# Optimization experiments

Measured on AMD Instinct MI355X. Metric: run time of the kernel, lower is better.

The kernel has to match this reference:

```python
import jax, jax.numpy as jnp
import numpy as np

# SSMBlock constants (from init_kwargs and standard mamba_ssm defaults)
W = 8            # pooled spatial edge; d_model = W^3
K = 16           # AvgPool3d kernel & stride
D_MODEL = W ** 3            # 512
D_STATE = 16
EXPAND = 2
D_INNER = EXPAND * D_MODEL  # 1024
DT_RANK = D_MODEL // 16     # 32 (ceil(512/16))
D_CONV = 4


def setup_inputs() -> dict:
    key = jax.random.key(0)
    ks = jax.random.split(key, 8)
    s = 0.02
    x = jax.random.normal(ks[0], (1, 64, 128, 128, 128), dtype=jnp.float32)
    in_proj_w = jax.random.normal(ks[1], (2 * D_INNER, D_MODEL), jnp.float32) * s
    conv_w = jax.random.normal(ks[2], (D_INNER, D_CONV), jnp.float32) * s
    conv_b = jnp.zeros((D_INNER,), jnp.float32)
    x_proj_w = jax.random.normal(ks[3], (DT_RANK + 2 * D_STATE, D_INNER), jnp.float32) * s
    dt_proj_w = jax.random.normal(ks[4], (D_INNER, DT_RANK), jnp.float32) * s
    dt_proj_b = jax.random.uniform(ks[5], (D_INNER,), jnp.float32, minval=-4.0, maxval=-2.0)
    A_log = jnp.log(jnp.broadcast_to(jnp.arange(1, D_STATE + 1, dtype=jnp.float32), (D_INNER, D_STATE)))
    D = jnp.ones((D_INNER,), jnp.float32)
    out_proj_w = jax.random.normal(ks[6], (D_MODEL, D_INNER), jnp.float32) * s
    return dict(x=x, in_proj_w=in_proj_w, conv_w=conv_w, conv_b=conv_b,
                x_proj_w=x_proj_w, dt_proj_w=dt_proj_w, dt_proj_b=dt_proj_b,
                A_log=A_log, D=D, out_proj_w=out_proj_w)


def _forward(x, in_proj_w, conv_w, conv_b, x_proj_w, dt_proj_w, dt_proj_b, A_log, D, out_proj_w):
    B, C = x.shape[0], x.shape[1]
    # AvgPool3d(K, stride=K): non-overlapping -> reshape + mean
    xp = x.reshape(B, C, W, K, W, K, W, K).mean(axis=(3, 5, 7))  # (B,C,W,W,W)
    seq = xp.reshape(B, C, D_MODEL)  # Mamba input: L = C, d_model = W^3

    # in_proj -> (x, z)
    xz = jnp.einsum('bld,ed->ble', seq, in_proj_w)  # (B,L,2*D_INNER)
    xs, z = jnp.split(xz, 2, axis=-1)

    # causal depthwise conv1d along L + SiLU
    xt = jnp.pad(xs, ((0, 0), (D_CONV - 1, 0), (0, 0))).transpose(0, 2, 1)  # (B,E,L+pad)
    conv = jax.lax.conv_general_dilated(
        xt, conv_w[:, None, :], window_strides=(1,), padding='VALID',
        dimension_numbers=('NCH', 'OIH', 'NCH'), feature_group_count=D_INNER)
    xs = jax.nn.silu(conv.transpose(0, 2, 1) + conv_b)  # (B,L,E)

    # input-dependent dt, B, C
    x_dbl = jnp.einsum('ble,fe->blf', xs, x_proj_w)
    dt, Bs, Cs = jnp.split(x_dbl, [DT_RANK, DT_RANK + D_STATE], axis=-1)
    dt = jax.nn.softplus(jnp.einsum('blr,er->ble', dt, dt_proj_w) + dt_proj_b)  # (B,L,E)

    # selective scan: h_t = exp(dt*A) h_{t-1} + (dt*x) B_t ; y_t = <h_t, C_t> + D*x_t
    A = -jnp.exp(A_log)                                  # (E,S)
    dA = jnp.exp(dt[..., None] * A)                      # (B,L,E,S)
    dBx = (dt * xs)[..., None] * Bs[:, :, None, :]       # (B,L,E,S)

    def step(h, inp):
        da, dbx, c = inp
        h = da * h + dbx                                 # (B,E,S)
        y = jnp.einsum('bes,bs->be', h, c)
        return h, y

    h0 = jnp.zeros((B, D_INNER, D_STATE), xs.dtype)
    _, ys = jax.lax.scan(step, h0, (dA.transpose(1, 0, 2, 3), dBx.transpose(1, 0, 2, 3), Cs.transpose(1, 0, 2)))
    y = ys.transpose(1, 0, 2) + xs * D                   # (B,L,E)

    y = y * jax.nn.silu(z)
    out = jnp.einsum('ble,de->bld', y, out_proj_w)       # (B,L,d_model)
    return out.reshape(B, C, W, W, W)


def reference(x, in_proj_w, conv_w, conv_b, x_proj_w, dt_proj_w, dt_proj_b, A_log, D, out_proj_w):
    return _forward(x, in_proj_w, conv_w, conv_b, x_proj_w, dt_proj_w, dt_proj_b, A_log, D, out_proj_w)
```

## Files before the change

kernel.cpp:

```cpp
#include <hip/hip_runtime.h>
#include <math.h>

typedef float f32x4 __attribute__((ext_vector_type(4)));

__device__ __forceinline__ float dot4v(f32x4 a, f32x4 b){
    return a.x*b.x + a.y*b.y + a.z*b.z + a.w*b.w;
}
__device__ __forceinline__ float dot4(float4 a, float4 b){
    return a.x*b.x + a.y*b.y + a.z*b.z + a.w*b.w;
}

__device__ __forceinline__ float reduce4(float a0, float a1, float a2, float a3, int lane){
    int b0 = lane & 1, b1 = lane & 2;
    float r  = b0 ? a1 : a0;
    float rt = b0 ? a0 : a1;
    r += __shfl_xor(rt, 1);
    float s  = b0 ? a3 : a2;
    float st = b0 ? a2 : a3;
    s += __shfl_xor(st, 1);
    float u  = b1 ? s : r;
    float ut = b1 ? r : s;
    u += __shfl_xor(ut, 2);
    u += __shfl_xor(u, 4);
    u += __shfl_xor(u, 8);
    u += __shfl_xor(u, 16);
    u += __shfl_xor(u, 32);
    return u;
}

__global__ __launch_bounds__(256) void pool_k(const float* __restrict__ x,
                                              float* __restrict__ seq){
    __shared__ float red[4][8];
    int tid  = threadIdx.x;
    int lane = tid & 63;
    int part = tid >> 6;
    int cdh  = blockIdx.x;
    int c  = cdh >> 6;
    int od = (cdh >> 3) & 7;
    int oh = cdh & 7;
    int half = lane >> 5;
    int f    = lane & 31;

    const f32x4* px = (const f32x4*)x;
    size_t base = ((size_t)(c * 128 + od * 16) * 128 + (size_t)(oh * 16 + half)) * 32 + f
                + (size_t)part * 4 * 4096;

    float acc = 0.f;
    #pragma unroll
    for (int ii = 0; ii < 4; ii++){
        size_t o = base + (size_t)ii * 4096;
        #pragma unroll
        for (int jj = 0; jj < 8; jj++){
            f32x4 v = __builtin_nontemporal_load(&px[o + (size_t)jj * 64]);
            acc += (v.x + v.y) + (v.z + v.w);
        }
    }
    acc += __shfl_xor(acc, 1);
    acc += __shfl_xor(acc, 2);
    acc += __shfl_xor(acc, 32);
    if (lane < 32 && (lane & 3) == 0) red[part][lane >> 2] = acc;
    __syncthreads();
    if (tid < 8){
        float v = red[0][tid] + red[1][tid] + red[2][tid] + red[3][tid];
        seq[c * 512 + od * 64 + oh * 8 + tid] = v * (1.0f / 4096.0f);
    }
}

__global__ __launch_bounds__(256) void inproj_k(const float* __restrict__ seq,
                                                const float* __restrict__ Win,
                                                float* __restrict__ xz){
    int lane = threadIdx.x & 63;
    int wid  = blockIdx.x * 4 + (threadIdx.x >> 6);
    int l0 = (wid >> 7) << 3;
    int e0 = (wid & 127) << 4;
    const f32x4* S = (const f32x4*)seq;
    f32x4 sa[8], sb[8];
    #pragma unroll
    for (int r = 0; r < 8; r++){
        sa[r] = S[(size_t)(l0 + r) * 128 + lane];
        sb[r] = S[(size_t)(l0 + r) * 128 + lane + 64];
    }
    #pragma unroll 2
    for (int j = 0; j < 16; j++){
        int e = e0 + j;
        const f32x4* W = (const f32x4*)Win + (size_t)e * 128;
        f32x4 w0 = W[lane], w1 = W[lane + 64];
        float a[8];
        #pragma unroll
        for (int r = 0; r < 8; r++) a[r] = dot4v(w0, sa[r]) + dot4v(w1, sb[r]);
        float u0 = reduce4(a[0], a[1], a[2], a[3], lane);
        float u1 = reduce4(a[4], a[5], a[6], a[7], lane);
        if (lane < 4){
            xz[(size_t)(l0 + lane) * 2048 + e]     = u0;
            xz[(size_t)(l0 + 4 + lane) * 2048 + e] = u1;
        }
    }
}

__global__ __launch_bounds__(1024) void cxp_k(const float* __restrict__ xz,
                                              const float* __restrict__ cw,
                                              const float* __restrict__ cb,
                                              const float* __restrict__ Wx,
                                              float* __restrict__ xsT,
                                              float* __restrict__ zsT,
                                              float* __restrict__ bcT,
                                              float* __restrict__ xdT){
    __shared__ float xs_row[1024];
    int l = blockIdx.x;
    int t = threadIdx.x;

    {
        int e = t;
        float v = cb[e];
        #pragma unroll
        for (int tt = 0; tt < 4; tt++){
            int ll = l - 3 + tt;
            if (ll >= 0) v += cw[e * 4 + tt] * xz[(size_t)ll * 2048 + e];
        }
        v = v / (1.f + expf(-v));
        xs_row[e] = v;
        xsT[(size_t)e * 64 + l] = v;
        float zv = xz[(size_t)l * 2048 + 1024 + e];
        zsT[(size_t)e * 64 + l] = zv / (1.f + expf(-zv));
    }
    __syncthreads();

    {
        int f = t >> 4, q = t & 15;
        const float4* X  = (const float4*)xs_row;
        const float4* W4 = (const float4*)(Wx + (size_t)f * 1024);
        float acc = 0.f;
        #pragma unroll
        for (int k4 = 0; k4 < 16; k4++){
            int idx = q * 16 + k4;
            acc += dot4(X[idx], W4[idx]);
        }
        acc += __shfl_xor(acc, 1);
        acc += __shfl_xor(acc, 2);
        acc += __shfl_xor(acc, 4);
        acc += __shfl_xor(acc, 8);
        if (q == 0){
            if (f < 32) xdT[(size_t)f * 64 + l] = acc;
            else        bcT[(size_t)(f - 32) * 64 + l] = acc;
        }
    }
}

__global__ __launch_bounds__(256) void scan_k(const float* __restrict__ xdT,
                                              const float* __restrict__ bcT,
                                              const float* __restrict__ xsT,
                                              const float* __restrict__ zsT,
                                              const float* __restrict__ Wdt,
                                              const float* __restrict__ bdt,
                                              const float* __restrict__ A_log,
                                              const float* __restrict__ Dv,
                                              float* __restrict__ y){
    __shared__ float red[4][64];
    int e    = blockIdx.x;
    int lane = threadIdx.x & 63;
    int w    = threadIdx.x >> 6;

    float acc = bdt[e];
    #pragma unroll 8
    for (int k = 0; k < 32; k++) acc += xdT[k * 64 + lane] * Wdt[e * 32 + k];
    float dtv = (acc > 20.f) ? acc : log1pf(expf(acc));
    float xv  = xsT[(size_t)e * 64 + lane];

    float py = 0.f;
    #pragma unroll
    for (int i = 0; i < 4; i++){
        int s = w * 4 + i;
        float A = -expf(A_log[e * 16 + s]);
        float a = expf(dtv * A);
        float b = (dtv * xv) * bcT[s * 64 + lane];
        #pragma unroll
        for (int d = 1; d < 64; d <<= 1){
            float ap = __shfl_up(a, d);
            float bp = __shfl_up(b, d);
            if (lane >= d){ b += a * bp; a *= ap; }
        }
        py += b * bcT[(16 + s) * 64 + lane];
    }
    red[w][lane] = py;
    __syncthreads();
    if (threadIdx.x < 64){
        float tot = red[0][lane] + red[1][lane] + red[2][lane] + red[3][lane];
        float yv = (tot + xv * Dv[e]) * zsT[(size_t)e * 64 + lane];
        y[(size_t)lane * 1024 + e] = yv;
    }
}

__global__ __launch_bounds__(256) void outproj_k(const float* __restrict__ y,
                                                 const float* __restrict__ Wo,
                                                 float* __restrict__ out){
    int lane = threadIdx.x & 63;
    int wid  = blockIdx.x * 4 + (threadIdx.x >> 6);
    int l0 = (wid >> 5) << 2;
    int d0 = (wid & 31) << 4;
    const float4* Y = (const float4*)y;
    float4 y0[4], y1[4], y2[4], y3[4];
    #pragma unroll
    for (int q = 0; q < 4; q++){
        y0[q] = Y[(size_t)(l0+0)*256 + q*64 + lane];
        y1[q] = Y[(size_t)(l0+1)*256 + q*64 + lane];
        y2[q] = Y[(size_t)(l0+2)*256 + q*64 + lane];
        y3[q] = Y[(size_t)(l0+3)*256 + q*64 + lane];
    }
    #pragma unroll 2
    for (int j = 0; j < 16; j++){
        int d = d0 + j;
        const float4* W = (const float4*)Wo + (size_t)d * 256;
        float a0 = 0.f, a1 = 0.f, a2 = 0.f, a3 = 0.f;
        #pragma unroll
        for (int q = 0; q < 4; q++){
            float4 w = W[q * 64 + lane];
            a0 += dot4(w, y0[q]);
            a1 += dot4(w, y1[q]);
            a2 += dot4(w, y2[q]);
            a3 += dot4(w, y3[q]);
        }
        float u = reduce4(a0, a1, a2, a3, lane);
        if (lane < 4) out[(size_t)(l0 + lane) * 512 + d] = u;
    }
}

extern "C" void kernel_launch(void* const* d_in, const int* in_sizes, int n_in,
                              void* d_out, int out_size, void* d_ws, size_t ws_size,
                              hipStream_t stream){
    const float* x          = (const float*)d_in[0];
    const float* in_proj_w  = (const float*)d_in[1];
    const float* conv_w     = (const float*)d_in[2];
    const float* conv_b     = (const float*)d_in[3];
    const float* x_proj_w   = (const float*)d_in[4];
    const float* dt_proj_w  = (const float*)d_in[5];
    const float* dt_proj_b  = (const float*)d_in[6];
    const float* A_log      = (const float*)d_in[7];
    const float* Dv         = (const float*)d_in[8];
    const float* out_proj_w = (const float*)d_in[9];
    float* out = (float*)d_out;

    float* ws   = (float*)d_ws;
    float* seq  = ws;
    float* xz   = ws + 32768;
    float* xsT  = ws + 163840;
    float* zsT  = ws + 229376;
    float* bcT  = ws + 294912;
    float* xdT  = ws + 296960;
    float* y    = ws + 299008;

    hipLaunchKernelGGL(pool_k,    dim3(4096), dim3(256),  0, stream, x, seq);
    hipLaunchKernelGGL(inproj_k,  dim3(256),  dim3(256),  0, stream, seq, in_proj_w, xz);
    hipLaunchKernelGGL(cxp_k,     dim3(64),   dim3(1024), 0, stream, xz, conv_w, conv_b,
                       x_proj_w, xsT, zsT, bcT, xdT);
    hipLaunchKernelGGL(scan_k,    dim3(1024), dim3(256),  0, stream, xdT, bcT, xsT, zsT,
                       dt_proj_w, dt_proj_b, A_log, Dv, y);
    hipLaunchKernelGGL(outproj_k, dim3(128),  dim3(256),  0, stream, y, out_proj_w, out);
}
```

Baseline: 126.8 us.

## Increase grid parallelism for small GEMMs and split conv/x_proj kernel

The fused conv+x_proj kernel ran on only 64 blocks. It is now split into a conv kernel (256 blocks) that also writes an L-major copy of xs, and a separate x_proj kernel (256 blocks). The in_proj and out_proj kernels give each wave fewer output columns so they launch 4x and 2x more blocks, and the pool load drops the nontemporal hint. The aim is to fill more CUs during the small GEMM stages, at the cost of one extra launch, an extra workspace buffer, and reloading seq and y rows per wave.

```diff
diff --git a/kernel.cpp b/kernel.cpp
--- a/kernel.cpp
+++ b/kernel.cpp
@@ -51,7 +51,7 @@
         size_t o = base + (size_t)ii * 4096;
         #pragma unroll
         for (int jj = 0; jj < 8; jj++){
-            f32x4 v = __builtin_nontemporal_load(&px[o + (size_t)jj * 64]);
+            f32x4 v = px[o + (size_t)jj * 64];
             acc += (v.x + v.y) + (v.z + v.w);
         }
     }
@@ -66,13 +66,13 @@
     }
 }
 
-__global__ __launch_bounds__(256) void inproj_k(const float* __restrict__ seq,
-                                                const float* __restrict__ Win,
-                                                float* __restrict__ xz){
+__global__ __launch_bounds__(256, 4) void inproj_k(const float* __restrict__ seq,
+                                                   const float* __restrict__ Win,
+                                                   float* __restrict__ xz){
     int lane = threadIdx.x & 63;
     int wid  = blockIdx.x * 4 + (threadIdx.x >> 6);
-    int l0 = (wid >> 7) << 3;
-    int e0 = (wid & 127) << 4;
+    int l0 = (wid >> 9) << 3;
+    int e0 = (wid & 511) << 2;
     const f32x4* S = (const f32x4*)seq;
     f32x4 sa[8], sb[8];
     #pragma unroll
@@ -80,8 +80,8 @@
         sa[r] = S[(size_t)(l0 + r) * 128 + lane];
         sb[r] = S[(size_t)(l0 + r) * 128 + lane + 64];
     }
-    #pragma unroll 2
-    for (int j = 0; j < 16; j++){
+    #pragma unroll
+    for (int j = 0; j < 4; j++){
         int e = e0 + j;
         const f32x4* W = (const f32x4*)Win + (size_t)e * 128;
         f32x4 w0 = W[lane], w1 = W[lane + 64];
@@ -97,52 +97,51 @@
     }
 }
 
-__global__ __launch_bounds__(1024) void cxp_k(const float* __restrict__ xz,
+__global__ __launch_bounds__(256) void conv_k(const float* __restrict__ xz,
                                               const float* __restrict__ cw,
                                               const float* __restrict__ cb,
-                                              const float* __restrict__ Wx,
                                               float* __restrict__ xsT,
                                               float* __restrict__ zsT,
-                                              float* __restrict__ bcT,
-                                              float* __restrict__ xdT){
-    __shared__ float xs_row[1024];
-    int l = blockIdx.x;
-    int t = threadIdx.x;
-
-    {
-        int e = t;
-        float v = cb[e];
-        #pragma unroll
-        for (int tt = 0; tt < 4; tt++){
-            int ll = l - 3 + tt;
-            if (ll >= 0) v += cw[e * 4 + tt] * xz[(size_t)ll * 2048 + e];
-        }
-        v = v / (1.f + expf(-v));
-        xs_row[e] = v;
-        xsT[(size_t)e * 64 + l] = v;
-        float zv = xz[(size_t)l * 2048 + 1024 + e];
-        zsT[(size_t)e * 64 + l] = zv / (1.f + expf(-zv));
-    }
-    __syncthreads();
-
-    {
-        int f = t >> 4, q = t & 15;
-        const float4* X  = (const float4*)xs_row;
-        const float4* W4 = (const float4*)(Wx + (size_t)f * 1024);
-        float acc = 0.f;
-        #pragma unroll
-        for (int k4 = 0; k4 < 16; k4++){
-            int idx = q * 16 + k4;
-            acc += dot4(X[idx], W4[idx]);
-        }
-        acc += __shfl_xor(acc, 1);
-        acc += __shfl_xor(acc, 2);
-        acc += __shfl_xor(acc, 4);
-        acc += __shfl_xor(acc, 8);
-        if (q == 0){
-            if (f < 32) xdT[(size_t)f * 64 + l] = acc;
-            else        bcT[(size_t)(f - 32) * 64 + l] = acc;
-        }
+                                              float* __restrict__ xsL){
+    int bid = blockIdx.x;
+    int l = bid >> 2;
+    int e = (bid & 3) * 256 + threadIdx.x;
+    float v = cb[e];
+    #pragma unroll
+    for (int tt = 0; tt < 4; tt++){
+        int ll = l - 3 + tt;
+        if (ll >= 0) v += cw[e * 4 + tt] * xz[(size_t)ll * 2048 + e];
+    }
+    v = v / (1.f + expf(-v));
+    xsT[(size_t)e * 64 + l] = v;
+    xsL[(size_t)l * 1024 + e] = v;
+    float zv = xz[(size_t)l * 2048 + 1024 + e];
+    zsT[(size_t)e * 64 + l] = zv / (1.f + expf(-zv));
+}
+
+__global__ __launch_bounds__(256) void xproj_k(const float* __restrict__ xsL,
+                                               const float* __restrict__ Wx,
+                                               float* __restrict__ bcT,
+                                               float* __restrict__ xdT){
+    int bid = blockIdx.x;
+    int l = bid >> 2;
+    int f = (bid & 3) * 16 + (threadIdx.x >> 4);
+    int q = threadIdx.x & 15;
+    const float4* X  = (const float4*)(xsL + (size_t)l * 1024);
+    const float4* W4 = (const float4*)(Wx + (size_t)f * 1024);
+    float acc = 0.f;
+    #pragma unroll
+    for (int k4 = 0; k4 < 16; k4++){
+        int idx = q * 16 + k4;
+        acc += dot4(X[idx], W4[idx]);
+    }
+    acc += __shfl_xor(acc, 1);
+    acc += __shfl_xor(acc, 2);
+    acc += __shfl_xor(acc, 4);
+    acc += __shfl_xor(acc, 8);
+    if (q == 0){
+        if (f < 32) xdT[(size_t)f * 64 + l] = acc;
+        else        bcT[(size_t)(f - 32) * 64 + l] = acc;
     }
 }
 
@@ -195,8 +194,8 @@
                                                  float* __restrict__ out){
     int lane = threadIdx.x & 63;
     int wid  = blockIdx.x * 4 + (threadIdx.x >> 6);
-    int l0 = (wid >> 5) << 2;
-    int d0 = (wid & 31) << 4;
+    int l0 = (wid >> 6) << 2;
+    int d0 = (wid & 63) << 3;
     const float4* Y = (const float4*)y;
     float4 y0[4], y1[4], y2[4], y3[4];
     #pragma unroll
@@ -207,7 +206,7 @@
         y3[q] = Y[(size_t)(l0+3)*256 + q*64 + lane];
     }
     #pragma unroll 2
-    for (int j = 0; j < 16; j++){
+    for (int j = 0; j < 8; j++){
         int d = d0 + j;
         const float4* W = (const float4*)Wo + (size_t)d * 256;
         float a0 = 0.f, a1 = 0.f, a2 = 0.f, a3 = 0.f;
@@ -244,15 +243,17 @@
     float* xz   = ws + 32768;
     float* xsT  = ws + 163840;
     float* zsT  = ws + 229376;
-    float* bcT  = ws + 294912;
-    float* xdT  = ws + 296960;
-    float* y    = ws + 299008;
-
-    hipLaunchKernelGGL(pool_k,    dim3(4096), dim3(256),  0, stream, x, seq);
-    hipLaunchKernelGGL(inproj_k,  dim3(256),  dim3(256),  0, stream, seq, in_proj_w, xz);
-    hipLaunchKernelGGL(cxp_k,     dim3(64),   dim3(1024), 0, stream, xz, conv_w, conv_b,
-                       x_proj_w, xsT, zsT, bcT, xdT);
-    hipLaunchKernelGGL(scan_k,    dim3(1024), dim3(256),  0, stream, xdT, bcT, xsT, zsT,
+    float* xsL  = ws + 294912;
+    float* bcT  = ws + 360448;
+    float* xdT  = ws + 362496;
+    float* y    = ws + 364544;
+
+    hipLaunchKernelGGL(pool_k,    dim3(4096), dim3(256), 0, stream, x, seq);
+    hipLaunchKernelGGL(inproj_k,  dim3(1024), dim3(256), 0, stream, seq, in_proj_w, xz);
+    hipLaunchKernelGGL(conv_k,    dim3(256),  dim3(256), 0, stream, xz, conv_w, conv_b,
+                       xsT, zsT, xsL);
+    hipLaunchKernelGGL(xproj_k,   dim3(256),  dim3(256), 0, stream, xsL, x_proj_w, bcT, xdT);
+    hipLaunchKernelGGL(scan_k,    dim3(1024), dim3(256), 0, stream, xdT, bcT, xsT, zsT,
                        dt_proj_w, dt_proj_b, A_log, Dv, y);
-    hipLaunchKernelGGL(outproj_k, dim3(128),  dim3(256),  0, stream, y, out_proj_w, out);
-}
+    hipLaunchKernelGGL(outproj_k, dim3(256),  dim3(256), 0, stream, y, out_proj_w, out);
+}
```

Result: no change. 129.3 us (+1.9%).
